# Kernel optimization log

Hardware: AMD Instinct MI355X
Metric: run time of the kernel (lower is better)

The kernel has to match this reference:

```python
import jax, jax.numpy as jnp
import numpy as np

B, N, D_MODEL, LAP = 64, 64, 256, 16


def setup_inputs() -> dict:
    key = jax.random.key(0)
    ks = jax.random.split(key, 8)
    adj = jax.random.randint(ks[0], (B, N, N), 0, 2, dtype=jnp.int32)
    node_feats = jax.random.normal(ks[1], (B, N, D_MODEL), dtype=jnp.float32)
    eigvec = jax.random.normal(ks[2], (B, N, LAP), dtype=jnp.float32)
    W_lap = jax.random.normal(ks[3], (LAP, D_MODEL), dtype=jnp.float32) / np.sqrt(LAP)
    W_edge = jax.random.normal(ks[4], (1 + 2 * LAP, D_MODEL), dtype=jnp.float32) / np.sqrt(1 + 2 * LAP)
    b_edge = jax.random.normal(ks[5], (D_MODEL,), dtype=jnp.float32) * 0.02
    type_embed = jax.random.normal(ks[6], (2, D_MODEL), dtype=jnp.float32)
    graph_tok = jax.random.normal(ks[7], (1, 1, D_MODEL), dtype=jnp.float32)
    return {"adj": adj, "node_feats": node_feats, "eigvec": eigvec,
            "W_lap": W_lap, "W_edge": W_edge, "b_edge": b_edge,
            "type_embed": type_embed, "graph_tok": graph_tok}


def reference(adj, node_feats, eigvec, W_lap, W_edge, b_edge, type_embed, graph_tok):
    b, n, _ = adj.shape
    d = graph_tok.shape[-1]
    # node tokens: feats + LapPE projection
    node_tok = node_feats + jnp.einsum('bnl,ld->bnd', eigvec, W_lap)
    # upper-triangular candidate edges (fixed M = n(n-1)/2, jit-friendly)
    iu, ju = jnp.triu_indices(n, k=1)               # [M]
    valid = adj[:, iu, ju] > 0                       # [B, M]
    # stable compaction: valid edges first (matches torch per-graph extraction order)
    order = jnp.argsort(~valid, axis=1, stable=True) # [B, M]
    src = iu[order]                                  # [B, M]
    dst = ju[order]
    valid_sorted = jnp.take_along_axis(valid, order, axis=1)
    Pu = jnp.take_along_axis(eigvec, src[..., None], axis=1)  # [B, M, LAP]
    Pv = jnp.take_along_axis(eigvec, dst[..., None], axis=1)
    m = src.shape[1]
    edge_in = jnp.concatenate([jnp.ones((b, m, 1), eigvec.dtype), Pu, Pv], axis=-1)
    etok = jnp.einsum('bmf,fd->bmd', edge_in, W_edge) + b_edge + type_embed[1]
    etok = jnp.where(valid_sorted[..., None], etok, 0.0)      # zeros at padding
    pad_mask_edges = ~valid_sorted                             # True = padding
    gtok = jnp.broadcast_to(graph_tok, (b, 1, d))
    seq_embeds = jnp.concatenate([gtok, node_tok, etok], axis=1)  # [B, 1+n+M, d]
    pad_mask = jnp.concatenate([jnp.zeros((b, 1 + n), bool), pad_mask_edges], axis=1)
    return seq_embeds, pad_mask
```

## Files before the change

### kernel.cpp

```cpp
#include <hip/hip_runtime.h>

#define B_ 64
#define N_ 64
#define D_ 256
#define LAP_ 16
#define M_ 2016
#define TOK_ 2081

typedef float v4f __attribute__((ext_vector_type(4)));

__device__ __forceinline__ void ij_from_m(int m, int& i, int& j) {
    float fm = (float)m;
    int gi = (int)((127.0f - sqrtf(127.0f * 127.0f - 8.0f * fm)) * 0.5f);
    if (gi < 0) gi = 0;
    if (gi > 62) gi = 62;
    while (gi > 0 && (127 * gi - gi * gi) / 2 > m) gi--;
    while (gi < 62 && (127 * (gi + 1) - (gi + 1) * (gi + 1)) / 2 <= m) gi++;
    i = gi;
    j = gi + 1 + (m - (127 * gi - gi * gi) / 2);
}

__global__ __launch_bounds__(256, 2) void prep_kernel(
    const int*   __restrict__ adj,
    const float* __restrict__ node_feats,
    const float* __restrict__ eigvec,
    const float* __restrict__ W_lap,
    const float* __restrict__ W_edge,
    const float* __restrict__ b_edge,
    const float* __restrict__ type_embed,
    const float* __restrict__ graph_tok,
    float*       __restrict__ out,
    float*       __restrict__ wsf,
    int*         __restrict__ src)
{
    const int b    = blockIdx.x;
    const int role = blockIdx.y;
    const int t    = threadIdx.x;
    const int wave = t >> 6, lane = t & 63;

    if (role == 0) {
        __shared__ int sAdj[N_ * N_];
        __shared__ unsigned long long sWords[32];
        __shared__ int sPref[32];
        __shared__ int sTotal;

#pragma unroll
        for (int r = 0; r < 4; r++)
            ((int4*)sAdj)[r * 256 + t] =
                ((const int4*)(adj + (size_t)b * (N_ * N_)))[r * 256 + t];
        __syncthreads();

#pragma unroll
        for (int k = 0; k < 8; k++) {
            int m = k * 256 + t;
            int valid = 0;
            if (m < M_) {
                int i, j;
                ij_from_m(m, i, j);
                valid = (sAdj[i * N_ + j] > 0) ? 1 : 0;
            }
            unsigned long long blt = __ballot(valid);
            if (lane == 0) sWords[k * 4 + wave] = blt;
        }
        __syncthreads();

        if (t < 32) {
            int cnt = __popcll(sWords[t]);
            int inc = cnt;
#pragma unroll
            for (int off = 1; off < 32; off <<= 1) {
                int v = __shfl_up(inc, off);
                if (lane >= off) inc += v;
            }
            sPref[t] = inc - cnt;
            if (t == 31) sTotal = inc;
        }
        __syncthreads();

        const int total = sTotal;
        float* maskb = out + (size_t)B_ * TOK_ * D_ + (size_t)b * TOK_;
#pragma unroll
        for (int k = 0; k < 8; k++) {
            int m = k * 256 + t;
            if (m < M_) {
                int w = m >> 6, r = m & 63;
                unsigned long long word = sWords[w];
                int rank = sPref[w] + __popcll(word & ((1ull << r) - 1ull));
                int valid = (int)((word >> r) & 1ull);
                int p = valid ? rank : total + (m - rank);
                int i, j;
                ij_from_m(m, i, j);
                src[b * M_ + p] = i | (j << 6) | (valid << 12);
                maskb[1 + N_ + p] = valid ? 0.0f : 1.0f;
            }
        }
        if (t < 1 + N_) maskb[t] = 0.0f;
        return;
    }

    __shared__ float sEig[N_ * LAP_];
    ((float4*)sEig)[t] = ((const float4*)(eigvec + (size_t)b * N_ * LAP_))[t];

    if (role <= 8) {
        const int isV = (role >= 5);
        const int n0  = (isV ? (role - 5) : (role - 1)) * 16;
        const float* Wsel = isV ? (W_edge + (1 + LAP_) * D_) : (W_edge + D_);
        float wc[LAP_];
#pragma unroll
        for (int l = 0; l < LAP_; l++) wc[l] = Wsel[l * D_ + t];
        __syncthreads();

        float* Tb = wsf + 256 + (size_t)b * N_ * D_
                  + (isV ? (size_t)B_ * N_ * D_ : 0);
#pragma unroll 4
        for (int k = 0; k < 16; k++) {
            int n = n0 + k;
            const float* e = sEig + n * LAP_;
            float acc = 0.0f;
#pragma unroll
            for (int l = 0; l < LAP_; l++) acc += e[l] * wc[l];
            Tb[n * D_ + t] = acc;
        }
        return;
    }

    float wlc[LAP_];
#pragma unroll
    for (int l = 0; l < LAP_; l++) wlc[l] = W_lap[l * D_ + t];
    __syncthreads();

    const int r9 = role - 9;
    const int n0 = r9 * 9;
    const int n1 = (r9 == 6) ? 64 : n0 + 9;
    float* outB = out + (size_t)b * TOK_ * D_;
    for (int n = n0; n < n1; n++) {
        float a = node_feats[((size_t)b * N_ + n) * D_ + t];
        const float* e = sEig + n * LAP_;
#pragma unroll
        for (int l = 0; l < LAP_; l++) a += e[l] * wlc[l];
        outB[(size_t)(1 + n) * D_ + t] = a;
    }
    if (role == 9) {
        outB[t] = graph_tok[t];
        if (b == 0)
            wsf[t] = W_edge[t] + b_edge[t] + type_embed[D_ + t];
    }
}

__global__ __launch_bounds__(256, 8) void edge_kernel(
    const float* __restrict__ wsf,
    const int*   __restrict__ src,
    float*       __restrict__ out)
{
    const int bid  = blockIdx.x;
    const int xcd  = bid & 7;
    const int idx  = bid >> 3;
    const int b    = ((idx & 7) << 3) | xcd;
    const int s    = idx >> 3;
    const int wave = threadIdx.x >> 6, lane = threadIdx.x & 63;

    v4f base4 = ((const v4f*)wsf)[lane];
    const float* Ub = wsf + 256 + (size_t)b * N_ * D_;
    const float* Vb = Ub + (size_t)B_ * N_ * D_;
    const int* sb = src + b * M_;
    float* outE = out + (size_t)b * TOK_ * D_ + (size_t)(1 + N_) * D_;

    const int p0 = s * 63;
    const int q15 = lane & 15;
    const int nq  = (63 - wave + 3) >> 2;
    int myinfo = (wave + 4 * q15 < 63) ? sb[p0 + wave + 4 * q15] : 0;

#pragma unroll 4
    for (int q = 0; q < nq; q++) {
        int info = __shfl(myinfo, q);
        int p = p0 + wave + 4 * q;
        v4f val = {0.0f, 0.0f, 0.0f, 0.0f};
        if (info & (1 << 12)) {
            int si = info & 63, di = (info >> 6) & 63;
            v4f u = ((const v4f*)(Ub + si * D_))[lane];
            v4f v = ((const v4f*)(Vb + di * D_))[lane];
            val = base4 + u + v;
        }
        ((v4f*)(outE + (size_t)p * D_))[lane] = val;
    }
}

extern "C" void kernel_launch(void* const* d_in, const int* in_sizes, int n_in,
                              void* d_out, int out_size, void* d_ws, size_t ws_size,
                              hipStream_t stream) {
    const int*   adj        = (const int*)d_in[0];
    const float* node_feats = (const float*)d_in[1];
    const float* eigvec     = (const float*)d_in[2];
    const float* W_lap      = (const float*)d_in[3];
    const float* W_edge     = (const float*)d_in[4];
    const float* b_edge     = (const float*)d_in[5];
    const float* type_embed = (const float*)d_in[6];
    const float* graph_tok  = (const float*)d_in[7];
    float* out = (float*)d_out;

    float* wsf = (float*)d_ws;
    int*   src = (int*)(wsf + 256 + 2 * (size_t)B_ * N_ * D_);

    prep_kernel<<<dim3(B_, 16), dim3(256), 0, stream>>>(
        adj, node_feats, eigvec, W_lap, W_edge, b_edge, type_embed, graph_tok,
        out, wsf, src);
    edge_kernel<<<dim3(2048), dim3(256), 0, stream>>>(wsf, src, out);
}
```

Baseline: 163.9 us.

## Fuse prep and edge kernels into one cooperative kernel with grid sync

Merges the two-kernel pipeline into a single cooperative kernel of 2048 blocks. Blocks first do compaction, the U/V projections or the node tokens, then synchronise across the grid and write the edge tokens. The compacted index array is no longer stored: each edge block recomputes its rank from ballot words and prefix sums kept in workspace, and writes the mask inline. The aim is to remove the second launch and the src round-trip. In exchange it adds a grid-wide barrier, needs all 2048 blocks resident at once (8 per CU via launch bounds), and falls back to the old path if the cooperative launch fails.

```diff
diff --git a/kernel.cpp b/kernel.cpp
--- a/kernel.cpp
+++ b/kernel.cpp
@@ -1,4 +1,7 @@
 #include <hip/hip_runtime.h>
+#include <hip/hip_cooperative_groups.h>
+
+namespace cg = cooperative_groups;
 
 #define B_ 64
 #define N_ 64
@@ -20,7 +23,146 @@
     j = gi + 1 + (m - (127 * gi - gi * gi) / 2);
 }
 
-__global__ __launch_bounds__(256, 2) void prep_kernel(
+__global__ __launch_bounds__(256, 8) void fused_kernel(
+    const int*   __restrict__ adj,
+    const float* __restrict__ node_feats,
+    const float* __restrict__ eigvec,
+    const float* __restrict__ W_lap,
+    const float* __restrict__ W_edge,
+    const float* __restrict__ b_edge,
+    const float* __restrict__ type_embed,
+    const float* __restrict__ graph_tok,
+    float*       __restrict__ out,
+    unsigned long long* __restrict__ wwords,
+    int*         __restrict__ wpref,
+    int*         __restrict__ wtotal,
+    float*       __restrict__ Uall,
+    float*       __restrict__ Vall)
+{
+    __shared__ char smem[16 * 1024 + 512];
+
+    const int bid  = blockIdx.x;
+    const int b    = bid & 63;
+    const int s    = bid >> 6;
+    const int t    = threadIdx.x;
+    const int wave = t >> 6, lane = t & 63;
+
+    if (s == 0) {
+        int* sAdj = (int*)smem;
+        unsigned long long* sW = (unsigned long long*)(smem + 16 * 1024);
+#pragma unroll
+        for (int r = 0; r < 4; r++)
+            ((int4*)sAdj)[r * 256 + t] =
+                ((const int4*)(adj + (size_t)b * (N_ * N_)))[r * 256 + t];
+        __syncthreads();
+#pragma unroll
+        for (int k = 0; k < 8; k++) {
+            int m = k * 256 + t;
+            int valid = 0;
+            if (m < M_) {
+                int i, j;
+                ij_from_m(m, i, j);
+                valid = (sAdj[i * N_ + j] > 0) ? 1 : 0;
+            }
+            unsigned long long blt = __ballot(valid);
+            if (lane == 0) sW[k * 4 + wave] = blt;
+        }
+        __syncthreads();
+        if (t < 32) {
+            unsigned long long word = sW[t];
+            int cnt = __popcll(word);
+            int inc = cnt;
+#pragma unroll
+            for (int off = 1; off < 32; off <<= 1) {
+                int v = __shfl_up(inc, off);
+                if (lane >= off) inc += v;
+            }
+            wwords[b * 32 + t] = word;
+            wpref [b * 32 + t] = inc - cnt;
+            if (t == 31) wtotal[b] = inc;
+        }
+    } else if (s <= 16) {
+        float* sEig = (float*)smem;
+        ((float4*)sEig)[t] = ((const float4*)(eigvec + (size_t)b * N_ * LAP_))[t];
+        const int isV = (s >= 9);
+        const int n0  = (isV ? (s - 9) : (s - 1)) * 8;
+        const float* Wsel = isV ? (W_edge + (1 + LAP_) * D_) : (W_edge + D_);
+        float wc[LAP_];
+#pragma unroll
+        for (int l = 0; l < LAP_; l++) wc[l] = Wsel[l * D_ + t];
+        __syncthreads();
+        float* Tb = (isV ? Vall : Uall) + (size_t)b * N_ * D_;
+#pragma unroll
+        for (int k = 0; k < 8; k++) {
+            int n = n0 + k;
+            const float* e = sEig + n * LAP_;
+            float acc = 0.0f;
+#pragma unroll
+            for (int l = 0; l < LAP_; l++) acc += e[l] * wc[l];
+            Tb[n * D_ + t] = acc;
+        }
+    } else {
+        float* sEig = (float*)smem;
+        ((float4*)sEig)[t] = ((const float4*)(eigvec + (size_t)b * N_ * LAP_))[t];
+        float wlc[LAP_];
+#pragma unroll
+        for (int l = 0; l < LAP_; l++) wlc[l] = W_lap[l * D_ + t];
+        __syncthreads();
+        const int r  = s - 17;
+        const int n0 = (r * 64) / 15, n1 = ((r + 1) * 64) / 15;
+        float* outB = out + (size_t)b * TOK_ * D_;
+        for (int n = n0; n < n1; n++) {
+            float a = node_feats[((size_t)b * N_ + n) * D_ + t];
+            const float* e = sEig + n * LAP_;
+#pragma unroll
+            for (int l = 0; l < LAP_; l++) a += e[l] * wlc[l];
+            outB[(size_t)(1 + n) * D_ + t] = a;
+        }
+        if (s == 17) {
+            outB[t] = graph_tok[t];
+            float* maskb = out + (size_t)B_ * TOK_ * D_ + (size_t)b * TOK_;
+            if (t < 1 + N_) maskb[t] = 0.0f;
+        }
+    }
+
+    cg::this_grid().sync();
+
+    v4f base4 = ((const v4f*)W_edge)[lane];
+    base4 += ((const v4f*)b_edge)[lane];
+    base4 += ((const v4f*)(type_embed + D_))[lane];
+
+    const float* Ub = Uall + (size_t)b * N_ * D_;
+    const float* Vb = Vall + (size_t)b * N_ * D_;
+    unsigned long long myword = (lane < 32) ? wwords[b * 32 + lane] : 0ull;
+    int mypref = (lane < 32) ? wpref[b * 32 + lane] : 0;
+    const int total = wtotal[b];
+    float* outE  = out + (size_t)b * TOK_ * D_ + (size_t)(1 + N_) * D_;
+    float* maskb = out + (size_t)B_ * TOK_ * D_ + (size_t)b * TOK_;
+
+    const int m0 = s * 63;
+#pragma unroll 4
+    for (int q = wave; q < 63; q += 4) {
+        int m = m0 + q;
+        int w = m >> 6, rr = m & 63;
+        unsigned long long word = __shfl(myword, w);
+        int pw = __shfl(mypref, w);
+        int rank = pw + __popcll(word & ((1ull << rr) - 1ull));
+        int valid = (int)((word >> rr) & 1ull);
+        int p = valid ? rank : total + (m - rank);
+        v4f val = {0.0f, 0.0f, 0.0f, 0.0f};
+        if (valid) {
+            int i, j;
+            ij_from_m(m, i, j);
+            v4f u = ((const v4f*)(Ub + i * D_))[lane];
+            v4f v = ((const v4f*)(Vb + j * D_))[lane];
+            val = base4 + u + v;
+        }
+        ((v4f*)(outE + (size_t)p * D_))[lane] = val;
+        if (lane == 0) maskb[1 + N_ + p] = valid ? 0.0f : 1.0f;
+    }
+}
+
+__global__ __launch_bounds__(256, 2) void prep_kernel_fb(
     const int*   __restrict__ adj,
     const float* __restrict__ node_feats,
     const float* __restrict__ eigvec,
@@ -43,13 +185,11 @@
         __shared__ unsigned long long sWords[32];
         __shared__ int sPref[32];
         __shared__ int sTotal;
-
 #pragma unroll
         for (int r = 0; r < 4; r++)
             ((int4*)sAdj)[r * 256 + t] =
                 ((const int4*)(adj + (size_t)b * (N_ * N_)))[r * 256 + t];
         __syncthreads();
-
 #pragma unroll
         for (int k = 0; k < 8; k++) {
             int m = k * 256 + t;
@@ -63,7 +203,6 @@
             if (lane == 0) sWords[k * 4 + wave] = blt;
         }
         __syncthreads();
-
         if (t < 32) {
             int cnt = __popcll(sWords[t]);
             int inc = cnt;
@@ -76,7 +215,6 @@
             if (t == 31) sTotal = inc;
         }
         __syncthreads();
-
         const int total = sTotal;
         float* maskb = out + (size_t)B_ * TOK_ * D_ + (size_t)b * TOK_;
 #pragma unroll
@@ -109,7 +247,6 @@
 #pragma unroll
         for (int l = 0; l < LAP_; l++) wc[l] = Wsel[l * D_ + t];
         __syncthreads();
-
         float* Tb = wsf + 256 + (size_t)b * N_ * D_
                   + (isV ? (size_t)B_ * N_ * D_ : 0);
 #pragma unroll 4
@@ -128,7 +265,6 @@
 #pragma unroll
     for (int l = 0; l < LAP_; l++) wlc[l] = W_lap[l * D_ + t];
     __syncthreads();
-
     const int r9 = role - 9;
     const int n0 = r9 * 9;
     const int n1 = (r9 == 6) ? 64 : n0 + 9;
@@ -147,7 +283,7 @@
     }
 }
 
-__global__ __launch_bounds__(256, 8) void edge_kernel(
+__global__ __launch_bounds__(256, 8) void edge_kernel_fb(
     const float* __restrict__ wsf,
     const int*   __restrict__ src,
     float*       __restrict__ out)
@@ -198,11 +334,32 @@
     const float* graph_tok  = (const float*)d_in[7];
     float* out = (float*)d_out;
 
-    float* wsf = (float*)d_ws;
-    int*   src = (int*)(wsf + 256 + 2 * (size_t)B_ * N_ * D_);
-
-    prep_kernel<<<dim3(B_, 16), dim3(256), 0, stream>>>(
-        adj, node_feats, eigvec, W_lap, W_edge, b_edge, type_embed, graph_tok,
-        out, wsf, src);
-    edge_kernel<<<dim3(2048), dim3(256), 0, stream>>>(wsf, src, out);
-}
+    unsigned long long* wwords = (unsigned long long*)d_ws;
+    int*   wpref  = (int*)((char*)d_ws + 16 * 1024);
+    int*   wtotal = (int*)((char*)d_ws + 24 * 1024);
+    float* Uall   = (float*)((char*)d_ws + 32 * 1024);
+    float* Vall   = Uall + (size_t)B_ * N_ * D_;
+
+    int dev = 0, coop = 0;
+    hipGetDevice(&dev);
+    hipDeviceGetAttribute(&coop, hipDeviceAttributeCooperativeLaunch, dev);
+
+    hipError_t err = hipErrorUnknown;
+    if (coop) {
+        void* args[] = {(void*)&adj, (void*)&node_feats, (void*)&eigvec,
+                        (void*)&W_lap, (void*)&W_edge, (void*)&b_edge,
+                        (void*)&type_embed, (void*)&graph_tok, (void*)&out,
+                        (void*)&wwords, (void*)&wpref, (void*)&wtotal,
+                        (void*)&Uall, (void*)&Vall};
+        err = hipLaunchCooperativeKernel((const void*)fused_kernel,
+                                         dim3(2048), dim3(256), args, 0, stream);
+    }
+    if (err != hipSuccess) {
+        float* wsf = (float*)d_ws;
+        int*   src = (int*)(wsf + 256 + 2 * (size_t)B_ * N_ * D_);
+        prep_kernel_fb<<<dim3(B_, 16), dim3(256), 0, stream>>>(
+            adj, node_feats, eigvec, W_lap, W_edge, b_edge, type_embed,
+            graph_tok, out, wsf, src);
+        edge_kernel_fb<<<dim3(2048), dim3(256), 0, stream>>>(wsf, src, out);
+    }
+}
```

Result: slower. 454.5 us (+177.3%).

## Move edge compaction scatter and pad-mask writes into edge kernel

Applied to the files above, without the earlier changes.

The prep kernel now stores only per-graph ballot words, word prefix sums and totals. The edge kernel recomputes each edge's compacted position, its (i,j) indices and validity from those words, and writes the pad-mask entries itself. The base vector is built per block from W_edge, b_edge and type_embed instead of a workspace slot. This removes the serial scatter in the role-0 block and the src index array round trip. In exchange it adds index math in the edge kernel, changes the block-to-graph mapping (dropping the XCD-aware swizzle), and writes outputs in a scattered order.

```diff
diff --git a/kernel.cpp b/kernel.cpp
--- a/kernel.cpp
+++ b/kernel.cpp
@@ -26,12 +26,13 @@
     const float* __restrict__ eigvec,
     const float* __restrict__ W_lap,
     const float* __restrict__ W_edge,
-    const float* __restrict__ b_edge,
-    const float* __restrict__ type_embed,
     const float* __restrict__ graph_tok,
     float*       __restrict__ out,
-    float*       __restrict__ wsf,
-    int*         __restrict__ src)
+    unsigned long long* __restrict__ wwords,
+    int*         __restrict__ wpref,
+    int*         __restrict__ wtotal,
+    float*       __restrict__ Uall,
+    float*       __restrict__ Vall)
 {
     const int b    = blockIdx.x;
     const int role = blockIdx.y;
@@ -41,15 +42,11 @@
     if (role == 0) {
         __shared__ int sAdj[N_ * N_];
         __shared__ unsigned long long sWords[32];
-        __shared__ int sPref[32];
-        __shared__ int sTotal;
-
 #pragma unroll
         for (int r = 0; r < 4; r++)
             ((int4*)sAdj)[r * 256 + t] =
                 ((const int4*)(adj + (size_t)b * (N_ * N_)))[r * 256 + t];
         __syncthreads();
-
 #pragma unroll
         for (int k = 0; k < 8; k++) {
             int m = k * 256 + t;
@@ -63,38 +60,19 @@
             if (lane == 0) sWords[k * 4 + wave] = blt;
         }
         __syncthreads();
-
         if (t < 32) {
-            int cnt = __popcll(sWords[t]);
+            unsigned long long word = sWords[t];
+            int cnt = __popcll(word);
             int inc = cnt;
 #pragma unroll
             for (int off = 1; off < 32; off <<= 1) {
                 int v = __shfl_up(inc, off);
                 if (lane >= off) inc += v;
             }
-            sPref[t] = inc - cnt;
-            if (t == 31) sTotal = inc;
-        }
-        __syncthreads();
-
-        const int total = sTotal;
-        float* maskb = out + (size_t)B_ * TOK_ * D_ + (size_t)b * TOK_;
-#pragma unroll
-        for (int k = 0; k < 8; k++) {
-            int m = k * 256 + t;
-            if (m < M_) {
-                int w = m >> 6, r = m & 63;
-                unsigned long long word = sWords[w];
-                int rank = sPref[w] + __popcll(word & ((1ull << r) - 1ull));
-                int valid = (int)((word >> r) & 1ull);
-                int p = valid ? rank : total + (m - rank);
-                int i, j;
-                ij_from_m(m, i, j);
-                src[b * M_ + p] = i | (j << 6) | (valid << 12);
-                maskb[1 + N_ + p] = valid ? 0.0f : 1.0f;
-            }
-        }
-        if (t < 1 + N_) maskb[t] = 0.0f;
+            wwords[b * 32 + t] = word;
+            wpref [b * 32 + t] = inc - cnt;
+            if (t == 31) wtotal[b] = inc;
+        }
         return;
     }
 
@@ -110,8 +88,7 @@
         for (int l = 0; l < LAP_; l++) wc[l] = Wsel[l * D_ + t];
         __syncthreads();
 
-        float* Tb = wsf + 256 + (size_t)b * N_ * D_
-                  + (isV ? (size_t)B_ * N_ * D_ : 0);
+        float* Tb = (isV ? Vall : Uall) + (size_t)b * N_ * D_;
 #pragma unroll 4
         for (int k = 0; k < 16; k++) {
             int n = n0 + k;
@@ -142,46 +119,59 @@
     }
     if (role == 9) {
         outB[t] = graph_tok[t];
-        if (b == 0)
-            wsf[t] = W_edge[t] + b_edge[t] + type_embed[D_ + t];
+        float* maskb = out + (size_t)B_ * TOK_ * D_ + (size_t)b * TOK_;
+        if (t < 1 + N_) maskb[t] = 0.0f;
     }
 }
 
 __global__ __launch_bounds__(256, 8) void edge_kernel(
-    const float* __restrict__ wsf,
-    const int*   __restrict__ src,
+    const float* __restrict__ Uall,
+    const float* __restrict__ Vall,
+    const unsigned long long* __restrict__ wwords,
+    const int*   __restrict__ wpref,
+    const int*   __restrict__ wtotal,
+    const float* __restrict__ W_edge,
+    const float* __restrict__ b_edge,
+    const float* __restrict__ type_embed,
     float*       __restrict__ out)
 {
     const int bid  = blockIdx.x;
-    const int xcd  = bid & 7;
-    const int idx  = bid >> 3;
-    const int b    = ((idx & 7) << 3) | xcd;
-    const int s    = idx >> 3;
+    const int b    = bid & 63;
+    const int s    = bid >> 6;
     const int wave = threadIdx.x >> 6, lane = threadIdx.x & 63;
 
-    v4f base4 = ((const v4f*)wsf)[lane];
-    const float* Ub = wsf + 256 + (size_t)b * N_ * D_;
-    const float* Vb = Ub + (size_t)B_ * N_ * D_;
-    const int* sb = src + b * M_;
-    float* outE = out + (size_t)b * TOK_ * D_ + (size_t)(1 + N_) * D_;
-
-    const int p0 = s * 63;
-    const int q15 = lane & 15;
-    const int nq  = (63 - wave + 3) >> 2;
-    int myinfo = (wave + 4 * q15 < 63) ? sb[p0 + wave + 4 * q15] : 0;
-
+    v4f base4 = ((const v4f*)W_edge)[lane];
+    base4 += ((const v4f*)b_edge)[lane];
+    base4 += ((const v4f*)(type_embed + D_))[lane];
+
+    const float* Ub = Uall + (size_t)b * N_ * D_;
+    const float* Vb = Vall + (size_t)b * N_ * D_;
+    unsigned long long myword = (lane < 32) ? wwords[b * 32 + lane] : 0ull;
+    int mypref = (lane < 32) ? wpref[b * 32 + lane] : 0;
+    const int total = wtotal[b];
+    float* outE  = out + (size_t)b * TOK_ * D_ + (size_t)(1 + N_) * D_;
+    float* maskb = out + (size_t)B_ * TOK_ * D_ + (size_t)b * TOK_;
+
+    const int m0 = s * 63;
 #pragma unroll 4
-    for (int q = 0; q < nq; q++) {
-        int info = __shfl(myinfo, q);
-        int p = p0 + wave + 4 * q;
+    for (int q = wave; q < 63; q += 4) {
+        int m = m0 + q;
+        int w = m >> 6, rr = m & 63;
+        unsigned long long word = __shfl(myword, w);
+        int pw = __shfl(mypref, w);
+        int rank = pw + __popcll(word & ((1ull << rr) - 1ull));
+        int valid = (int)((word >> rr) & 1ull);
+        int p = valid ? rank : total + (m - rank);
         v4f val = {0.0f, 0.0f, 0.0f, 0.0f};
-        if (info & (1 << 12)) {
-            int si = info & 63, di = (info >> 6) & 63;
-            v4f u = ((const v4f*)(Ub + si * D_))[lane];
-            v4f v = ((const v4f*)(Vb + di * D_))[lane];
+        if (valid) {
+            int i, j;
+            ij_from_m(m, i, j);
+            v4f u = ((const v4f*)(Ub + i * D_))[lane];
+            v4f v = ((const v4f*)(Vb + j * D_))[lane];
             val = base4 + u + v;
         }
         ((v4f*)(outE + (size_t)p * D_))[lane] = val;
+        if (lane == 0) maskb[1 + N_ + p] = valid ? 0.0f : 1.0f;
     }
 }
 
@@ -198,11 +188,15 @@
     const float* graph_tok  = (const float*)d_in[7];
     float* out = (float*)d_out;
 
-    float* wsf = (float*)d_ws;
-    int*   src = (int*)(wsf + 256 + 2 * (size_t)B_ * N_ * D_);
+    unsigned long long* wwords = (unsigned long long*)d_ws;
+    int*   wpref  = (int*)((char*)d_ws + 16 * 1024);
+    int*   wtotal = (int*)((char*)d_ws + 24 * 1024);
+    float* Uall   = (float*)((char*)d_ws + 32 * 1024);
+    float* Vall   = Uall + (size_t)B_ * N_ * D_;
 
     prep_kernel<<<dim3(B_, 16), dim3(256), 0, stream>>>(
-        adj, node_feats, eigvec, W_lap, W_edge, b_edge, type_embed, graph_tok,
-        out, wsf, src);
-    edge_kernel<<<dim3(2048), dim3(256), 0, stream>>>(wsf, src, out);
-}
+        adj, node_feats, eigvec, W_lap, W_edge, graph_tok,
+        out, wwords, wpref, wtotal, Uall, Vall);
+    edge_kernel<<<dim3(2048), dim3(256), 0, stream>>>(
+        Uall, Vall, wwords, wpref, wtotal, W_edge, b_edge, type_embed, out);
+}
```

Measured after the change: 168.7 us. +2.9%, slower.
